# Kernel optimization log

Hardware: AMD Instinct MI355X
Metric: run time of the kernel (lower is better)

## Reference

```python
import jax, jax.numpy as jnp
import numpy as np

VOCAB, NUM_TAGS, EMB, HID = 30000, 20, 200, 128
B, S = 128, 512


def setup_inputs() -> dict:
    key = jax.random.key(0)
    ks = jax.random.split(key, 13)
    sentence = jax.random.randint(ks[0], (B, S), 0, VOCAB)
    tags = jax.random.randint(ks[1], (B, S), 0, NUM_TAGS)
    lengths = jax.random.randint(ks[2], (B,), 1, S + 1)
    mask = jnp.arange(S)[None, :] < lengths[:, None]  # [B,S] bool, mask[:,0] all True
    sc = 0.1
    return {
        "sentence": sentence,
        "tags": tags,
        "mask": mask,
        "embedding": jax.random.normal(ks[3], (VOCAB, EMB), jnp.float32) * sc,
        "W_ih": jax.random.normal(ks[4], (4 * HID, EMB), jnp.float32) * sc,
        "W_hh": jax.random.normal(ks[5], (4 * HID, HID), jnp.float32) * sc,
        "b_ih": jax.random.normal(ks[6], (4 * HID,), jnp.float32) * sc,
        "b_hh": jax.random.normal(ks[7], (4 * HID,), jnp.float32) * sc,
        "W_dec": jax.random.normal(ks[8], (NUM_TAGS, HID), jnp.float32) * sc,
        "b_dec": jax.random.normal(ks[9], (NUM_TAGS,), jnp.float32) * sc,
        "start_trans": jax.random.normal(ks[10], (NUM_TAGS,), jnp.float32) * sc,
        "end_trans": jax.random.normal(ks[11], (NUM_TAGS,), jnp.float32) * sc,
        "trans": jax.random.normal(ks[12], (NUM_TAGS, NUM_TAGS), jnp.float32) * sc,
    }


def _lstm(embeds, W_ih, W_hh, b_ih, b_hh):
    # torch nn.LSTM, single layer, batch_first, zero init state; gate order i,f,g,o
    b = embeds.shape[0]
    h0 = jnp.zeros((b, HID), embeds.dtype)
    x = jnp.swapaxes(embeds, 0, 1)  # [S,B,E]
    xg = jnp.einsum('sbe,ge->sbg', x, W_ih) + b_ih + b_hh  # input projections, [S,B,4H]

    def step(carry, xg_t):
        h, c = carry
        g = xg_t + h @ W_hh.T
        i, f, gg, o = jnp.split(g, 4, axis=-1)
        c = jax.nn.sigmoid(f) * c + jax.nn.sigmoid(i) * jnp.tanh(gg)
        h = jax.nn.sigmoid(o) * jnp.tanh(c)
        return (h, c), h

    _, hs = jax.lax.scan(step, (h0, h0), xg)
    return jnp.swapaxes(hs, 0, 1)  # [B,S,H]


def _crf_nll_mean(emissions, tags, mask, start_trans, end_trans, trans):
    # torchcrf.CRF negative log likelihood, reduction='mean' (mean over batch)
    b = emissions.shape[0]
    ems = jnp.swapaxes(emissions, 0, 1)          # [S,B,T]
    tgs = jnp.swapaxes(tags, 0, 1)               # [S,B]
    msk = jnp.swapaxes(mask, 0, 1).astype(emissions.dtype)  # [S,B]
    bidx = jnp.arange(b)

    # numerator: score of the gold path
    num0 = start_trans[tgs[0]] + ems[0, bidx, tgs[0]]

    def nstep(score, inp):
        em, tag, ptag, m = inp
        return score + (trans[ptag, tag] + em[bidx, tag]) * m, None

    num, _ = jax.lax.scan(nstep, num0, (ems[1:], tgs[1:], tgs[:-1], msk[1:]))
    last_idx = mask.sum(axis=1).astype(jnp.int32) - 1
    num = num + end_trans[tags[bidx, last_idx]]

    # denominator: forward algorithm (log partition)
    sc0 = start_trans[None, :] + ems[0]  # [B,T]

    def dstep(score, inp):
        em, m = inp
        nxt = jax.nn.logsumexp(score[:, :, None] + trans[None] + em[:, None, :], axis=1)
        return jnp.where(m[:, None] > 0, nxt, score), None

    sc, _ = jax.lax.scan(dstep, sc0, (ems[1:], msk[1:]))
    den = jax.nn.logsumexp(sc + end_trans[None, :], axis=1)
    return -jnp.mean(num - den)


def reference(sentence, tags, mask, embedding, W_ih, W_hh, b_ih, b_hh,
              W_dec, b_dec, start_trans, end_trans, trans):
    embeds = embedding[sentence]                           # [B,S,E]
    lstm_out = _lstm(embeds, W_ih, W_hh, b_ih, b_hh)       # [B,S,H]
    emissions = jnp.einsum('bsh,th->bst', lstm_out, W_dec) + b_dec  # [B,S,T]
    # dropout treated as identity (eval-mode reference)
    return _crf_nll_mean(emissions, tags, mask, start_trans, end_trans, trans)
```

## Files before the change

### kernel.cpp

```cpp
#include <hip/hip_runtime.h>
#include <hip/hip_bf16.h>
#include <hip/hip_fp16.h>
#include <math.h>

#define B_ 128
#define S_ 512
#define EMB_ 200
#define HID_ 128
#define NT_ 20
#define G4_ 512
#define KP_ 224

typedef _Float16 f16x2_t __attribute__((ext_vector_type(2)));
typedef short bf16x8 __attribute__((ext_vector_type(8)));
typedef float f32x4 __attribute__((ext_vector_type(4)));

#if __has_builtin(__builtin_amdgcn_fdot2)
#define FDOT2(a, b, c) __builtin_amdgcn_fdot2(__builtin_bit_cast(f16x2_t, (a)), \
                                              __builtin_bit_cast(f16x2_t, (b)), (c), false)
#else
static __device__ __forceinline__ float fdot2_fb(unsigned a, unsigned b, float c) {
    float alo = __half2float(__ushort_as_half((unsigned short)(a & 0xffffu)));
    float ahi = __half2float(__ushort_as_half((unsigned short)(a >> 16)));
    float blo = __half2float(__ushort_as_half((unsigned short)(b & 0xffffu)));
    float bhi = __half2float(__ushort_as_half((unsigned short)(b >> 16)));
    return c + alo * blo + ahi * bhi;
}
#define FDOT2(a, b, c) fdot2_fb((a), (b), (c))
#endif

__device__ __forceinline__ float bf2f(unsigned u) {
    union { unsigned u; float f; } cv;
    cv.u = u << 16;
    return cv.f;
}
__device__ __forceinline__ unsigned packh2(float a, float b) {
    return ((unsigned)__half_as_ushort(__float2half(b)) << 16)
         | (unsigned)__half_as_ushort(__float2half(a));
}
__device__ __forceinline__ unsigned short f2bf(float f) {
    __hip_bfloat16 h = __float2bfloat16(f);
    unsigned short u;
    __builtin_memcpy(&u, &h, 2);
    return u;
}

__global__ void k_detect(const unsigned char* mask, int* flag) {
    __shared__ int partial[4];
    int tid = threadIdx.x;
    int s = 0;
    for (int i = tid; i < B_ * S_; i += 256) {
        if (i & 3) s += mask[i];
    }
    for (int m = 32; m >= 1; m >>= 1) s += __shfl_xor(s, m);
    if ((tid & 63) == 0) partial[tid >> 6] = s;
    __syncthreads();
    if (tid == 0) {
        int tot = partial[0] + partial[1] + partial[2] + partial[3];
        flag[0] = (tot > 0) ? 1 : 0;
    }
}

__global__ void k_prep(const float* __restrict__ W_ih, const float* __restrict__ b_ih,
                       const float* __restrict__ b_hh, __hip_bfloat16* __restrict__ Wb,
                       float* __restrict__ biasb) {
    int i = blockIdx.x * 256 + threadIdx.x;
    if (i < G4_ * KP_) {
        int g = i / KP_, k = i - g * KP_;
        float v = (k < EMB_) ? W_ih[g * EMB_ + k] : 0.f;
        Wb[i] = __float2bfloat16(v);
    }
    if (i < G4_) biasb[i] = b_ih[i] + b_hh[i];
}

__global__ __launch_bounds__(256, 2) void k_xg(const int* __restrict__ sentence,
                                               const float* __restrict__ embedding,
                                               const __hip_bfloat16* __restrict__ Wb,
                                               const float* __restrict__ biasb,
                                               __hip_bfloat16* __restrict__ xg) {
    __shared__ short Bl[G4_ * 40];
    __shared__ short Al[32 * 40];
    __shared__ int ids_s[32];
    int tid = threadIdx.x;
    int m0 = blockIdx.x * 32;
    int lane = tid & 63;
    int gbase = (tid >> 6) * 128;
    if (tid < 32) ids_s[tid] = sentence[m0 + tid];
    __syncthreads();

    f32x4 acc0[8], acc1[8];
#pragma unroll
    for (int n = 0; n < 8; n++) {
        acc0[n] = (f32x4){0.f, 0.f, 0.f, 0.f};
        acc1[n] = (f32x4){0.f, 0.f, 0.f, 0.f};
    }
    int lrow = lane & 15, lk = lane >> 4;

    for (int c = 0; c < 7; c++) {
        int k0 = c * 32;
#pragma unroll
        for (int i = 0; i < 8; i++) {
            int idx = tid + 256 * i;
            int row = idx >> 2, q = idx & 3;
            uint4 v = *(const uint4*)((const short*)Wb + (size_t)row * KP_ + k0 + q * 8);
            *(uint4*)(Bl + row * 40 + q * 8) = v;
        }
#pragma unroll
        for (int i = 0; i < 2; i++) {
            int j = tid + 256 * i;
            int row = j >> 4, kp = j & 15;
            int k = k0 + kp * 2;
            const float* e = embedding + (size_t)ids_s[row] * EMB_;
            float v0 = (k < EMB_) ? e[k] : 0.f;
            float v1 = (k + 1 < EMB_) ? e[k + 1] : 0.f;
            unsigned u = (unsigned)f2bf(v0) | ((unsigned)f2bf(v1) << 16);
            *(unsigned*)(Al + row * 40 + kp * 2) = u;
        }
        __syncthreads();
        bf16x8 a0 = *(const bf16x8*)(Al + lrow * 40 + lk * 8);
        bf16x8 a1 = *(const bf16x8*)(Al + (lrow + 16) * 40 + lk * 8);
#pragma unroll
        for (int n = 0; n < 8; n++) {
            bf16x8 bfr = *(const bf16x8*)(Bl + (gbase + n * 16 + lrow) * 40 + lk * 8);
            acc0[n] = __builtin_amdgcn_mfma_f32_16x16x32_bf16(a0, bfr, acc0[n], 0, 0, 0);
            acc1[n] = __builtin_amdgcn_mfma_f32_16x16x32_bf16(a1, bfr, acc1[n], 0, 0, 0);
        }
        __syncthreads();
    }
    int rbase = m0 + lk * 4;
#pragma unroll
    for (int n = 0; n < 8; n++) {
        int g = gbase + n * 16 + lrow;
        float bv = biasb[g];
#pragma unroll
        for (int r = 0; r < 4; r++) {
            xg[(size_t)(rbase + r) * G4_ + g] = __float2bfloat16(acc0[n][r] + bv);
            xg[(size_t)(rbase + r + 16) * G4_ + g] = __float2bfloat16(acc1[n][r] + bv);
        }
    }
}

__global__ __launch_bounds__(1024) __attribute__((amdgpu_waves_per_eu(4, 4)))
void k_lstm(const __hip_bfloat16* __restrict__ xg,
            const float* __restrict__ W_hh,
            unsigned* __restrict__ h2_out) {
    __shared__ unsigned h2_lds[64];
    __shared__ float part_lds[G4_];
    __shared__ float gate_lds[G4_];
    int b = blockIdx.x, tid = threadIdx.x;
    int wv = tid >> 6, lane = tid & 63;
    int p = wv >> 3;
    int g = ((wv & 7) << 6) | lane;

    unsigned w2[32];
    const float2* wrow = (const float2*)(W_hh + (size_t)g * HID_ + p * 64);
#pragma unroll
    for (int k = 0; k < 32; k++) {
        float2 f = wrow[k];
        w2[k] = packh2(f.x, f.y);
    }
#pragma unroll
    for (int k = 0; k < 32; k++) asm("" : "+v"(w2[k]));

    if (tid < 64) h2_lds[tid] = 0u;
    float c0 = 0.f, c1 = 0.f;
    const ushort* xgb = (const ushort*)(xg) + (size_t)b * S_ * G4_;
    unsigned* h2b = h2_out + (size_t)b * S_ * 64;
    __syncthreads();

    unsigned xr = (p == 0) ? (unsigned)xgb[g] : 0u;
    for (int t = 0; t < S_; t++) {
        unsigned xr_next = 0u;
        if (p == 0) {
            int tn = (t + 1 < S_) ? t + 1 : t;
            xr_next = xgb[(size_t)tn * G4_ + g];
        }
        float acc = 0.f;
        const uint4* hb4 = (const uint4*)(h2_lds + (p << 5));
#pragma unroll
        for (int q = 0; q < 8; q++) {
            uint4 hh = hb4[q];
            acc = FDOT2(w2[4 * q + 0], hh.x, acc);
            acc = FDOT2(w2[4 * q + 1], hh.y, acc);
            acc = FDOT2(w2[4 * q + 2], hh.z, acc);
            acc = FDOT2(w2[4 * q + 3], hh.w, acc);
        }
        if (p == 1) part_lds[g] = acc;
        __syncthreads();
        if (p == 0) {
            float pre = bf2f(xr) + acc + part_lds[g];
            int gt = g >> 7;
            float xs = (gt == 2) ? 2.f * pre : pre;
            xs = fminf(fmaxf(xs, -30.f), 30.f);
            float r = 1.f / (1.f + __expf(-xs));
            gate_lds[g] = (gt == 2) ? 2.f * r - 1.f : r;
        }
        __syncthreads();
        if (tid < 64) {
            int j = tid;
            float2 iv = *(const float2*)(gate_lds + 2 * j);
            float2 fv = *(const float2*)(gate_lds + 128 + 2 * j);
            float2 gv = *(const float2*)(gate_lds + 256 + 2 * j);
            float2 ov = *(const float2*)(gate_lds + 384 + 2 * j);
            c0 = fv.x * c0 + iv.x * gv.x;
            c1 = fv.y * c1 + iv.y * gv.y;
            float h0 = ov.x * (2.f / (1.f + __expf(-2.f * c0)) - 1.f);
            float h1 = ov.y * (2.f / (1.f + __expf(-2.f * c1)) - 1.f);
            unsigned pk = packh2(h0, h1);
            h2_lds[j] = pk;
            h2b[(size_t)t * 64 + j] = pk;
        }
        __syncthreads();
        xr = xr_next;
    }
}

__global__ __launch_bounds__(320) void k_em(const unsigned* __restrict__ h2,
                                            const float* __restrict__ W_dec,
                                            const float* __restrict__ b_dec,
                                            float* __restrict__ em) {
    int half = threadIdx.x / 160;
    int r = threadIdx.x % 160;
    int tag = r >> 3, l8 = r & 7;
    const float* wd = W_dec + tag * HID_ + l8 * 16;
    float ws[16];
#pragma unroll
    for (int q = 0; q < 16; q++) ws[q] = wd[q];
    float bd = b_dec[tag];
    int row0 = blockIdx.x * 16 + half * 8;
    for (int rp = 0; rp < 8; rp++) {
        int row = row0 + rp;
        const uint4* h4 = (const uint4*)(h2 + (size_t)row * 64 + l8 * 8);
        uint4 a = h4[0], bq = h4[1];
        unsigned hv[8] = {a.x, a.y, a.z, a.w, bq.x, bq.y, bq.z, bq.w};
        float pacc = 0.f;
#pragma unroll
        for (int q = 0; q < 8; q++) {
            float lo = __half2float(__ushort_as_half((unsigned short)(hv[q] & 0xffffu)));
            float hi = __half2float(__ushort_as_half((unsigned short)(hv[q] >> 16)));
            pacc += lo * ws[2 * q] + hi * ws[2 * q + 1];
        }
        pacc += __shfl_xor(pacc, 1);
        pacc += __shfl_xor(pacc, 2);
        pacc += __shfl_xor(pacc, 4);
        if (l8 == 0) em[(size_t)row * NT_ + tag] = pacc + bd;
    }
}

__global__ __launch_bounds__(64) void k_crf(const float* __restrict__ em,
                                            const int* __restrict__ tags,
                                            const void* __restrict__ mask,
                                            const int* __restrict__ flag,
                                            const float* __restrict__ start_trans,
                                            const float* __restrict__ end_trans,
                                            const float* __restrict__ trans,
                                            float* __restrict__ nll) {
    __shared__ float em_s[S_ * NT_];
    __shared__ float trans_s[NT_ * NT_];
    __shared__ int tags_s[S_];
    __shared__ unsigned char mask_s[S_];
    __shared__ __align__(16) float score_s[32];
    __shared__ float num_sh;

    int b = blockIdx.x;
    int lane = threadIdx.x;
    const float4* e4 = (const float4*)(em + (size_t)b * S_ * NT_);
    float4* s4 = (float4*)em_s;
    for (int i = lane; i < S_ * NT_ / 4; i += 64) s4[i] = e4[i];
    for (int i = lane; i < NT_ * NT_; i += 64) trans_s[i] = trans[i];
    for (int i = lane; i < S_; i += 64) tags_s[i] = tags[b * S_ + i];
    int fl = flag[0];
    for (int i = lane; i < S_; i += 64) {
        mask_s[i] = fl ? ((const unsigned char*)mask)[b * S_ + i]
                       : (unsigned char)(((const int*)mask)[b * S_ + i] != 0);
    }
    __syncthreads();

    float nsum = 0.f;
    int cnt = 0;
    for (int t = lane; t < S_; t += 64) cnt += mask_s[t];
    for (int t = 1 + lane; t < S_; t += 64) {
        if (mask_s[t]) {
            int tg = tags_s[t], pt = tags_s[t - 1];
            nsum += trans_s[pt * NT_ + tg] + em_s[t * NT_ + tg];
        }
    }
    for (int m = 32; m >= 1; m >>= 1) {
        nsum += __shfl_xor(nsum, m);
        cnt += __shfl_xor(cnt, m);
    }
    if (lane == 0) {
        int t0 = tags_s[0];
        num_sh = nsum + start_trans[t0] + em_s[t0] + end_trans[tags_s[cnt - 1]];
    }

    int tag = (lane < NT_) ? lane : NT_ - 1;
    float tcol[NT_];
#pragma unroll
    for (int p = 0; p < NT_; p++) tcol[p] = trans_s[p * NT_ + tag];
    float sc = start_trans[tag] + em_s[tag];
    if (lane < NT_) score_s[lane] = sc;
    __syncthreads();

    for (int t = 1; t < S_; t++) {
        const float4* q4 = (const float4*)score_s;
        float4 q0 = q4[0], q1 = q4[1], q2 = q4[2], q3 = q4[3], q5 = q4[4];
        float v[NT_] = {q0.x + tcol[0],  q0.y + tcol[1],  q0.z + tcol[2],  q0.w + tcol[3],
                        q1.x + tcol[4],  q1.y + tcol[5],  q1.z + tcol[6],  q1.w + tcol[7],
                        q2.x + tcol[8],  q2.y + tcol[9],  q2.z + tcol[10], q2.w + tcol[11],
                        q3.x + tcol[12], q3.y + tcol[13], q3.z + tcol[14], q3.w + tcol[15],
                        q5.x + tcol[16], q5.y + tcol[17], q5.z + tcol[18], q5.w + tcol[19]};
        float mx[NT_];
#pragma unroll
        for (int p = 0; p < NT_; p++) mx[p] = v[p];
#pragma unroll
        for (int n = NT_; n > 1; n = (n + 1) >> 1) {
#pragma unroll
            for (int i = 0; i < (n >> 1); i++) mx[i] = fmaxf(mx[i], mx[n - 1 - i]);
        }
        float ex[NT_];
#pragma unroll
        for (int p = 0; p < NT_; p++) ex[p] = __expf(v[p] - mx[0]);
#pragma unroll
        for (int n = NT_; n > 1; n = (n + 1) >> 1) {
#pragma unroll
            for (int i = 0; i < (n >> 1); i++) ex[i] += ex[n - 1 - i];
        }
        float nxt = mx[0] + __logf(ex[0]) + em_s[t * NT_ + tag];
        sc = mask_s[t] ? nxt : sc;
        __syncthreads();
        if (lane < NT_) score_s[lane] = sc;
        __syncthreads();
    }

    if (lane < NT_) score_s[lane] = sc + end_trans[tag];
    __syncthreads();
    if (lane == 0) {
        float m = score_s[0];
#pragma unroll
        for (int i = 1; i < NT_; i++) m = fmaxf(m, score_s[i]);
        float s = 0.f;
#pragma unroll
        for (int i = 0; i < NT_; i++) s += __expf(score_s[i] - m);
        nll[b] = (m + __logf(s)) - num_sh;
    }
}

__global__ void k_final(const float* __restrict__ nll, float* __restrict__ out) {
    __shared__ float sums[2];
    int tid = threadIdx.x;
    float v = nll[tid];
    for (int m = 32; m >= 1; m >>= 1) v += __shfl_xor(v, m);
    if ((tid & 63) == 0) sums[tid >> 6] = v;
    __syncthreads();
    if (tid == 0) out[0] = (sums[0] + sums[1]) * (1.f / (float)B_);
}

extern "C" void kernel_launch(void* const* d_in, const int* in_sizes, int n_in,
                              void* d_out, int out_size, void* d_ws, size_t ws_size,
                              hipStream_t stream) {
    const int* sentence = (const int*)d_in[0];
    const int* tags = (const int*)d_in[1];
    const void* mask = d_in[2];
    const float* embedding = (const float*)d_in[3];
    const float* W_ih = (const float*)d_in[4];
    const float* W_hh = (const float*)d_in[5];
    const float* b_ih = (const float*)d_in[6];
    const float* b_hh = (const float*)d_in[7];
    const float* W_dec = (const float*)d_in[8];
    const float* b_dec = (const float*)d_in[9];
    const float* start_trans = (const float*)d_in[10];
    const float* end_trans = (const float*)d_in[11];
    const float* trans = (const float*)d_in[12];

    char* ws = (char*)d_ws;
    int* flag = (int*)ws;
    __hip_bfloat16* xg = (__hip_bfloat16*)(ws + 256);
    size_t off = 256 + (size_t)B_ * S_ * G4_ * 2;
    float* em = (float*)(ws + off);
    off += (size_t)B_ * S_ * NT_ * 4;
    float* nllp = (float*)(ws + off);
    off += 512;
    unsigned* h2_out = (unsigned*)(ws + off);
    off += (size_t)B_ * S_ * 64 * 4;
    __hip_bfloat16* Wb = (__hip_bfloat16*)(ws + off);
    off += (size_t)G4_ * KP_ * 2;
    float* biasb = (float*)(ws + off);

    k_detect<<<1, 256, 0, stream>>>((const unsigned char*)mask, flag);
    k_prep<<<(G4_ * KP_ + 255) / 256, 256, 0, stream>>>(W_ih, b_ih, b_hh, Wb, biasb);
    k_xg<<<(B_ * S_) / 32, 256, 0, stream>>>(sentence, embedding, Wb, biasb, xg);
    k_lstm<<<B_, 1024, 0, stream>>>(xg, W_hh, h2_out);
    k_em<<<(B_ * S_) / 16, 320, 0, stream>>>(h2_out, W_dec, b_dec, em);
    k_crf<<<B_, 64, 0, stream>>>(em, tags, mask, flag, start_trans, end_trans, trans, nllp);
    k_final<<<1, 128, 0, stream>>>(nllp, (float*)d_out);
}
```

Baseline: 709.9 us.

## Fuse emission projection into LSTM recurrence using idle waves

Computes the decoder emissions inside the LSTM kernel, using the upper 512 threads (otherwise idle during the gate phase) to dot the previous step's packed fp16 hidden state with fp16-packed W_dec. A final pass after the loop covers the last timestep. This removes the separate k_em launch and the round trip of the full hidden-state buffer through global memory. It adds work and register pressure to the latency-bound recurrent loop, and the decoder weights are now fp16 instead of fp32.

```diff
diff --git a/kernel.cpp b/kernel.cpp
--- a/kernel.cpp
+++ b/kernel.cpp
@@ -62,8 +62,9 @@
 }
 
 __global__ void k_prep(const float* __restrict__ W_ih, const float* __restrict__ b_ih,
-                       const float* __restrict__ b_hh, __hip_bfloat16* __restrict__ Wb,
-                       float* __restrict__ biasb) {
+                       const float* __restrict__ b_hh, const float* __restrict__ W_dec,
+                       __hip_bfloat16* __restrict__ Wb, float* __restrict__ biasb,
+                       unsigned* __restrict__ Wd2) {
     int i = blockIdx.x * 256 + threadIdx.x;
     if (i < G4_ * KP_) {
         int g = i / KP_, k = i - g * KP_;
@@ -71,6 +72,10 @@
         Wb[i] = __float2bfloat16(v);
     }
     if (i < G4_) biasb[i] = b_ih[i] + b_hh[i];
+    if (i < NT_ * 64) {
+        int tg = i >> 6, j = i & 63;
+        Wd2[i] = packh2(W_dec[tg * HID_ + 2 * j], W_dec[tg * HID_ + 2 * j + 1]);
+    }
 }
 
 __global__ __launch_bounds__(256, 2) void k_xg(const int* __restrict__ sentence,
@@ -143,7 +148,9 @@
 __global__ __launch_bounds__(1024) __attribute__((amdgpu_waves_per_eu(4, 4)))
 void k_lstm(const __hip_bfloat16* __restrict__ xg,
             const float* __restrict__ W_hh,
-            unsigned* __restrict__ h2_out) {
+            const unsigned* __restrict__ Wd2,
+            const float* __restrict__ b_dec,
+            float* __restrict__ em) {
     __shared__ unsigned h2_lds[64];
     __shared__ float part_lds[G4_];
     __shared__ float gate_lds[G4_];
@@ -162,10 +169,21 @@
 #pragma unroll
     for (int k = 0; k < 32; k++) asm("" : "+v"(w2[k]));
 
+    int ge = (tid >= 512) ? tid - 512 : 0;
+    bool isEm = (tid >= 512) && (ge < 320);
+    int tag = ge >> 4, l16 = ge & 15;
+    unsigned we[4] = {0u, 0u, 0u, 0u};
+    float bd = 0.f;
+    if (isEm) {
+        const unsigned* wdp = Wd2 + tag * 64 + l16 * 4;
+        we[0] = wdp[0]; we[1] = wdp[1]; we[2] = wdp[2]; we[3] = wdp[3];
+        bd = b_dec[tag];
+    }
+
     if (tid < 64) h2_lds[tid] = 0u;
     float c0 = 0.f, c1 = 0.f;
     const ushort* xgb = (const ushort*)(xg) + (size_t)b * S_ * G4_;
-    unsigned* h2b = h2_out + (size_t)b * S_ * 64;
+    float* emb = em + (size_t)b * S_ * NT_;
     __syncthreads();
 
     unsigned xr = (p == 0) ? (unsigned)xgb[g] : 0u;
@@ -184,6 +202,14 @@
             acc = FDOT2(w2[4 * q + 1], hh.y, acc);
             acc = FDOT2(w2[4 * q + 2], hh.z, acc);
             acc = FDOT2(w2[4 * q + 3], hh.w, acc);
+        }
+        float ep = 0.f;
+        if (isEm) {
+            uint4 eh = *(const uint4*)(h2_lds + l16 * 4);
+            ep = FDOT2(we[0], eh.x, ep);
+            ep = FDOT2(we[1], eh.y, ep);
+            ep = FDOT2(we[2], eh.z, ep);
+            ep = FDOT2(we[3], eh.w, ep);
         }
         if (p == 1) part_lds[g] = acc;
         __syncthreads();
@@ -194,6 +220,12 @@
             xs = fminf(fmaxf(xs, -30.f), 30.f);
             float r = 1.f / (1.f + __expf(-xs));
             gate_lds[g] = (gt == 2) ? 2.f * r - 1.f : r;
+        } else if (isEm && t > 0) {
+            ep += __shfl_xor(ep, 1);
+            ep += __shfl_xor(ep, 2);
+            ep += __shfl_xor(ep, 4);
+            ep += __shfl_xor(ep, 8);
+            if (l16 == 0) emb[(size_t)(t - 1) * NT_ + tag] = ep + bd;
         }
         __syncthreads();
         if (tid < 64) {
@@ -206,44 +238,23 @@
             c1 = fv.y * c1 + iv.y * gv.y;
             float h0 = ov.x * (2.f / (1.f + __expf(-2.f * c0)) - 1.f);
             float h1 = ov.y * (2.f / (1.f + __expf(-2.f * c1)) - 1.f);
-            unsigned pk = packh2(h0, h1);
-            h2_lds[j] = pk;
-            h2b[(size_t)t * 64 + j] = pk;
+            h2_lds[j] = packh2(h0, h1);
         }
         __syncthreads();
         xr = xr_next;
     }
-}
-
-__global__ __launch_bounds__(320) void k_em(const unsigned* __restrict__ h2,
-                                            const float* __restrict__ W_dec,
-                                            const float* __restrict__ b_dec,
-                                            float* __restrict__ em) {
-    int half = threadIdx.x / 160;
-    int r = threadIdx.x % 160;
-    int tag = r >> 3, l8 = r & 7;
-    const float* wd = W_dec + tag * HID_ + l8 * 16;
-    float ws[16];
-#pragma unroll
-    for (int q = 0; q < 16; q++) ws[q] = wd[q];
-    float bd = b_dec[tag];
-    int row0 = blockIdx.x * 16 + half * 8;
-    for (int rp = 0; rp < 8; rp++) {
-        int row = row0 + rp;
-        const uint4* h4 = (const uint4*)(h2 + (size_t)row * 64 + l8 * 8);
-        uint4 a = h4[0], bq = h4[1];
-        unsigned hv[8] = {a.x, a.y, a.z, a.w, bq.x, bq.y, bq.z, bq.w};
-        float pacc = 0.f;
-#pragma unroll
-        for (int q = 0; q < 8; q++) {
-            float lo = __half2float(__ushort_as_half((unsigned short)(hv[q] & 0xffffu)));
-            float hi = __half2float(__ushort_as_half((unsigned short)(hv[q] >> 16)));
-            pacc += lo * ws[2 * q] + hi * ws[2 * q + 1];
-        }
-        pacc += __shfl_xor(pacc, 1);
-        pacc += __shfl_xor(pacc, 2);
-        pacc += __shfl_xor(pacc, 4);
-        if (l8 == 0) em[(size_t)row * NT_ + tag] = pacc + bd;
+    if (isEm) {
+        uint4 eh = *(const uint4*)(h2_lds + l16 * 4);
+        float ep = 0.f;
+        ep = FDOT2(we[0], eh.x, ep);
+        ep = FDOT2(we[1], eh.y, ep);
+        ep = FDOT2(we[2], eh.z, ep);
+        ep = FDOT2(we[3], eh.w, ep);
+        ep += __shfl_xor(ep, 1);
+        ep += __shfl_xor(ep, 2);
+        ep += __shfl_xor(ep, 4);
+        ep += __shfl_xor(ep, 8);
+        if (l16 == 0) emb[(size_t)(S_ - 1) * NT_ + tag] = ep + bd;
     }
 }
 
@@ -381,17 +392,17 @@
     off += (size_t)B_ * S_ * NT_ * 4;
     float* nllp = (float*)(ws + off);
     off += 512;
-    unsigned* h2_out = (unsigned*)(ws + off);
-    off += (size_t)B_ * S_ * 64 * 4;
     __hip_bfloat16* Wb = (__hip_bfloat16*)(ws + off);
     off += (size_t)G4_ * KP_ * 2;
     float* biasb = (float*)(ws + off);
+    off += 2048;
+    unsigned* Wd2 = (unsigned*)(ws + off);
 
     k_detect<<<1, 256, 0, stream>>>((const unsigned char*)mask, flag);
-    k_prep<<<(G4_ * KP_ + 255) / 256, 256, 0, stream>>>(W_ih, b_ih, b_hh, Wb, biasb);
+    k_prep<<<(G4_ * KP_ + 255) / 256, 256, 0, stream>>>(W_ih, b_ih, b_hh, W_dec,
+                                                        Wb, biasb, Wd2);
     k_xg<<<(B_ * S_) / 32, 256, 0, stream>>>(sentence, embedding, Wb, biasb, xg);
-    k_lstm<<<B_, 1024, 0, stream>>>(xg, W_hh, h2_out);
-    k_em<<<(B_ * S_) / 16, 320, 0, stream>>>(h2_out, W_dec, b_dec, em);
+    k_lstm<<<B_, 1024, 0, stream>>>(xg, W_hh, Wd2, b_dec, em);
     k_crf<<<B_, 64, 0, stream>>>(em, tags, mask, flag, start_trans, end_trans, trans, nllp);
     k_final<<<1, 128, 0, stream>>>(nllp, (float*)d_out);
 }
```

After: 759.9 us. +7.0%, slower.
